# Kernel optimization log

Measured on AMD Instinct MI355X. Metric: run time of the kernel, lower is better.

Reference implementation:

```python
import jax, jax.numpy as jnp
import numpy as np

NUM_HEADS = 16


def setup_inputs() -> dict:
    key = jax.random.key(0)
    k1, k2, k3 = jax.random.split(key, 3)
    B, N, C = 4, 2048, 1024
    x = jax.random.normal(k1, (B, N, C), dtype=jnp.float32)
    w_qkv = jax.random.normal(k2, (C, 3 * C), dtype=jnp.float32) * (C ** -0.5)
    w_proj = jax.random.normal(k3, (C, C), dtype=jnp.float32) * (C ** -0.5)
    b_proj = jnp.zeros((C,), dtype=jnp.float32)
    return {"x": x, "w_qkv": w_qkv, "w_proj": w_proj, "b_proj": b_proj}


def reference(x, w_qkv, w_proj, b_proj):
    B, N, C = x.shape
    H = NUM_HEADS
    hd = C // H
    scale = hd ** -0.5
    # qkv projection (no bias), split into q, k, v per head
    qkv = jnp.einsum('bnc,cd->bnd', x, w_qkv)            # [B, N, 3C]
    qkv = qkv.reshape(B, N, 3, H, hd).transpose(0, 3, 2, 1, 4)  # [B, H, 3, N, hd]
    q, k, v = qkv[:, :, 0], qkv[:, :, 1], qkv[:, :, 2]   # each [B, H, N, hd]
    q = q * scale
    attn = jax.nn.softmax(jnp.einsum('bhnd,bhmd->bhnm', q, k), axis=-1)  # [B, H, N, N]
    out = jnp.einsum('bhnm,bhmd->bhnd', attn, v)         # [B, H, N, hd]
    out = out.transpose(0, 2, 1, 3).reshape(B, N, C)
    return jnp.einsum('bnc,cd->bnd', out, w_proj) + b_proj
```

## Files before the change

### kernel.cpp

```cpp
#include <hip/hip_runtime.h>

typedef short s16x8 __attribute__((ext_vector_type(8)));
typedef float f32x4 __attribute__((ext_vector_type(4)));
typedef float f32x16 __attribute__((ext_vector_type(16)));
typedef unsigned u32x4 __attribute__((ext_vector_type(4)));


__device__ __forceinline__ unsigned short bf16bits(float f) {
  unsigned u = __builtin_bit_cast(unsigned, f);
  unsigned rnd = 0x7FFFu + ((u >> 16) & 1u);
  return (unsigned short)((u + rnd) >> 16);
}

__device__ __forceinline__ unsigned pk_bf16(float lo, float hi) {
  unsigned r;
  asm("v_cvt_pk_bf16_f32 %0, %1, %2" : "=v"(r) : "v"(lo), "v"(hi));
  return r;
}

__device__ __forceinline__ void async16(const void* g, void* l) {
  __builtin_amdgcn_global_load_lds((const __attribute__((address_space(1))) void*)g,
                                   (__attribute__((address_space(3))) void*)l, 16, 0, 0);
}

__device__ __forceinline__ f32x4 mfma16(s16x8 a, s16x8 b, f32x4 c) {
  return __builtin_amdgcn_mfma_f32_16x16x32_bf16(a, b, c, 0, 0, 0);
}

__device__ __forceinline__ f32x16 mfma32(s16x8 a, s16x8 b, f32x16 c) {
  return __builtin_amdgcn_mfma_f32_32x32x16_bf16(a, b, c, 0, 0, 0);
}

__device__ __forceinline__ s16x8 lds_frag(const unsigned short* S, int row, int c8, int U) {
  int unit = row * U + (c8 ^ (row & (U - 1)));
  return *(const s16x8*)(S + unit * 8);
}


__global__ __launch_bounds__(256) void cvt_f32_bf16(const float4* __restrict__ in,
                                                    unsigned short* __restrict__ out, int n4) {
  int i = blockIdx.x * blockDim.x + threadIdx.x;
  int stride = gridDim.x * blockDim.x;
  for (; i < n4; i += stride) {
    float4 v = in[i];
    ushort4 o;
    o.x = bf16bits(v.x); o.y = bf16bits(v.y); o.z = bf16bits(v.z); o.w = bf16bits(v.w);
    *(ushort4*)(out + (size_t)i * 4) = o;
  }
}

__global__ __launch_bounds__(256) void transpose_f32_bf16(const float* __restrict__ in,
                                                          unsigned short* __restrict__ out,
                                                          int R, int C) {
  __shared__ float tile[32][33];
  int c0 = blockIdx.x * 32, r0 = blockIdx.y * 32;
  int tx = threadIdx.x, ty = threadIdx.y;
  #pragma unroll
  for (int i = 0; i < 32; i += 8)
    tile[ty + i][tx] = in[(size_t)(r0 + ty + i) * C + c0 + tx];
  __syncthreads();
  #pragma unroll
  for (int i = 0; i < 32; i += 8)
    out[(size_t)(c0 + ty + i) * R + r0 + tx] = bf16bits(tile[tx][ty + i]);
}


template <typename EPI>
__global__ __launch_bounds__(256) void gemm_bt(const unsigned short* __restrict__ A,
                                               const unsigned short* __restrict__ Bt,
                                               int K, EPI epi) {
  __shared__ __align__(16) unsigned short As[128 * 64];
  __shared__ __align__(16) unsigned short Bs[128 * 64];
  const int tid = threadIdx.x, wid = tid >> 6, lane = tid & 63;
  const int quad = lane >> 4, l16 = lane & 15;
  const int bm0 = blockIdx.y * 128, bn0 = blockIdx.x * 128;
  const int wm = (wid & 1) * 64, wn = (wid >> 1) * 64;
  f32x4 acc[4][4] = {};

  for (int kt = 0; kt < K; kt += 64) {
    #pragma unroll
    for (int t = 0; t < 4; ++t) {
      int c = wid * 4 + t;
      int u = c * 64 + lane;
      int row = u >> 3;
      int c8 = (u & 7) ^ (row & 7);
      async16(A + (size_t)(bm0 + row) * K + kt + c8 * 8, (char*)As + c * 1024);
      async16(Bt + (size_t)(bn0 + row) * K + kt + c8 * 8, (char*)Bs + c * 1024);
    }
    __syncthreads();
    #pragma unroll
    for (int kk = 0; kk < 2; ++kk) {
      s16x8 a[4], b[4];
      #pragma unroll
      for (int i = 0; i < 4; ++i) a[i] = lds_frag(As, wm + i * 16 + l16, kk * 4 + quad, 8);
      #pragma unroll
      for (int j = 0; j < 4; ++j) b[j] = lds_frag(Bs, wn + j * 16 + l16, kk * 4 + quad, 8);
      #pragma unroll
      for (int i = 0; i < 4; ++i)
        #pragma unroll
        for (int j = 0; j < 4; ++j)
          acc[i][j] = mfma16(a[i], b[j], acc[i][j]);
    }
    __syncthreads();
  }
  #pragma unroll
  for (int i = 0; i < 4; ++i)
    #pragma unroll
    for (int j = 0; j < 4; ++j) {
      int m0 = bm0 + wm + i * 16 + quad * 4;
      int n = bn0 + wn + j * 16 + l16;
      #pragma unroll
      for (int r = 0; r < 4; ++r) epi(m0 + r, n, acc[i][j][r]);
    }
}

struct QKVEpi {
  unsigned short *Q, *K, *Vt;
  float qscale;
  __device__ __forceinline__ void operator()(int m, int n, float v) const {
    int s = n >> 10, h = (n >> 6) & 15, d = n & 63;
    int b = m >> 11, ns = m & 2047;
    if (s == 2) {
      Vt[(((size_t)b * 16 + h) * 64 + d) * 2048 + ns] = bf16bits(v);
    } else {
      unsigned short* dst = s ? K : Q;
      float val = s ? v : v * qscale;
      dst[(((size_t)b * 16 + h) * 2048 + ns) * 64 + d] = bf16bits(val);
    }
  }
};

struct ProjEpi {
  const float* bias;
  float* out;
  __device__ __forceinline__ void operator()(int m, int n, float v) const {
    out[(size_t)m * 1024 + n] = v + bias[n];
  }
};

__global__ __launch_bounds__(256, 3) void flash_attn(const unsigned short* __restrict__ Q,
                                                     const unsigned short* __restrict__ K,
                                                     const unsigned short* __restrict__ Vt,
                                                     unsigned short* __restrict__ O) {
  __shared__ __align__(16) unsigned short Ks[2][64 * 64];
  __shared__ __align__(16) unsigned short Vs[2][64 * 64];
  const int tid = threadIdx.x, wid = tid >> 6, lane = tid & 63;
  const int l31 = lane & 31, half = lane >> 5;
  const int bh = blockIdx.y, qt = blockIdx.x;
  const unsigned short* Qg = Q + (size_t)bh * 2048 * 64;
  const unsigned short* Kg = K + (size_t)bh * 2048 * 64;
  const unsigned short* Vg = Vt + (size_t)bh * 64 * 2048;
  const int q0 = qt * 256 + wid * 64;

  s16x8 qB[2][4];
  #pragma unroll
  for (int g = 0; g < 2; ++g) {
    int qrow = q0 + g * 32 + l31;
    #pragma unroll
    for (int s = 0; s < 4; ++s)
      qB[g][s] = *(const s16x8*)&Qg[(size_t)qrow * 64 + s * 16 + half * 8];
  }

  const int c0 = wid * 2, c1 = wid * 2 + 1;
  const int u0 = c0 * 64 + lane, u1 = c1 * 64 + lane;
  const int kr0 = u0 >> 3, kc0 = ((u0 & 7) ^ (kr0 & 7)) * 8;
  const int kr1 = u1 >> 3, kc1 = ((u1 & 7) ^ (kr1 & 7)) * 8;

  auto stage = [&](int kt, int buf) {
    const int kb = kt * 64;
    async16(Kg + (size_t)(kb + kr0) * 64 + kc0, (char*)&Ks[buf][0] + c0 * 1024);
    async16(Kg + (size_t)(kb + kr1) * 64 + kc1, (char*)&Ks[buf][0] + c1 * 1024);
    async16(Vg + (size_t)kr0 * 2048 + kb + kc0, (char*)&Vs[buf][0] + c0 * 1024);
    async16(Vg + (size_t)kr1 * 2048 + kb + kc1, (char*)&Vs[buf][0] + c1 * 1024);
  };

  f32x16 oacc[2][2] = {};
  float l_i[2] = {0.f, 0.f};
  const f32x16 fz = {};

  stage(0, 0);
  for (int kt = 0; kt < 32; ++kt) {
    const int cur = kt & 1;
    __syncthreads();
    if (kt + 1 < 32) stage(kt + 1, cur ^ 1);
    const unsigned short* ks = &Ks[cur][0];
    const unsigned short* vs = &Vs[cur][0];

    #pragma unroll
    for (int kf = 0; kf < 2; ++kf) {
      f32x16 st[2];
      {
        s16x8 a = lds_frag(ks, kf * 32 + l31, half, 8);
        st[0] = mfma32(a, qB[0][0], fz);
        st[1] = mfma32(a, qB[1][0], fz);
      }
      #pragma unroll
      for (int s = 1; s < 4; ++s) {
        s16x8 a = lds_frag(ks, kf * 32 + l31, s * 2 + half, 8);
        st[0] = mfma32(a, qB[0][s], st[0]);
        st[1] = mfma32(a, qB[1][s], st[1]);
      }
      #pragma unroll
      for (int g = 0; g < 2; ++g) {
        float rs = 0.f;
        #pragma unroll
        for (int r = 0; r < 16; ++r) {
          float p = __builtin_amdgcn_exp2f(st[g][r]);
          st[g][r] = p;
          rs += p;
        }
        rs += __shfl_xor(rs, 32);
        l_i[g] += rs;
      }
      #pragma unroll
      for (int t = 0; t < 2; ++t) {
        int rb = t * 8;
        u32x4 bP[2];
        #pragma unroll
        for (int g = 0; g < 2; ++g) {
          unsigned pa0 = pk_bf16(st[g][rb + 0], st[g][rb + 1]);
          unsigned pa1 = pk_bf16(st[g][rb + 2], st[g][rb + 3]);
          unsigned pb0 = pk_bf16(st[g][rb + 4], st[g][rb + 5]);
          unsigned pb1 = pk_bf16(st[g][rb + 6], st[g][rb + 7]);
          unsigned s0 = half ? pa0 : pb0;
          unsigned s1 = half ? pa1 : pb1;
          unsigned r0 = (unsigned)__shfl_xor((int)s0, 32);
          unsigned r1 = (unsigned)__shfl_xor((int)s1, 32);
          bP[g][0] = half ? r0 : pa0;
          bP[g][1] = half ? r1 : pa1;
          bP[g][2] = half ? pb0 : r0;
          bP[g][3] = half ? pb1 : r1;
        }
        #pragma unroll
        for (int f = 0; f < 2; ++f) {
          s16x8 aV = lds_frag(vs, f * 32 + l31, (kf * 2 + t) * 2 + half, 8);
          oacc[0][f] = mfma32(aV, __builtin_bit_cast(s16x8, bP[0]), oacc[0][f]);
          oacc[1][f] = mfma32(aV, __builtin_bit_cast(s16x8, bP[1]), oacc[1][f]);
        }
      }
    }
  }

  const int b = bh >> 4, h = bh & 15;
  #pragma unroll
  for (int g = 0; g < 2; ++g) {
    float inv = 1.f / l_i[g];
    int qrow = q0 + g * 32 + l31;
    size_t base = (((size_t)b * 2048 + qrow) * 16 + h) * 64;
    #pragma unroll
    for (int f = 0; f < 2; ++f)
      #pragma unroll
      for (int q = 0; q < 4; ++q) {
        int d0 = f * 32 + q * 8 + half * 4;
        uint2 o;
        o.x = pk_bf16(oacc[g][f][q * 4 + 0] * inv, oacc[g][f][q * 4 + 1] * inv);
        o.y = pk_bf16(oacc[g][f][q * 4 + 2] * inv, oacc[g][f][q * 4 + 3] * inv);
        *(uint2*)&O[base + d0] = o;
      }
  }
}


extern "C" void kernel_launch(void* const* d_in, const int* in_sizes, int n_in,
                              void* d_out, int out_size, void* d_ws, size_t ws_size,
                              hipStream_t stream) {
  (void)in_sizes; (void)n_in; (void)out_size; (void)ws_size;
  const float* x = (const float*)d_in[0];
  const float* w_qkv = (const float*)d_in[1];
  const float* w_proj = (const float*)d_in[2];
  const float* b_proj = (const float*)d_in[3];
  float* out = (float*)d_out;
  char* ws = (char*)d_ws;
  const size_t MB = 1ull << 20;
  unsigned short* Xb  = (unsigned short*)(ws);
  unsigned short* Wqt = (unsigned short*)(ws + 16 * MB);
  unsigned short* Wpt = (unsigned short*)(ws + 22 * MB);
  unsigned short* Qb  = (unsigned short*)(ws + 24 * MB);
  unsigned short* Kb  = (unsigned short*)(ws + 40 * MB);
  unsigned short* Vt  = (unsigned short*)(ws + 56 * MB);
  unsigned short* Ob  = Xb;

  cvt_f32_bf16<<<2048, 256, 0, stream>>>((const float4*)x, Xb, 8388608 / 4);
  transpose_f32_bf16<<<dim3(96, 32), dim3(32, 8), 0, stream>>>(w_qkv, Wqt, 1024, 3072);
  transpose_f32_bf16<<<dim3(32, 32), dim3(32, 8), 0, stream>>>(w_proj, Wpt, 1024, 1024);

  QKVEpi e1{Qb, Kb, Vt, 0.125f * 1.44269504088896340736f};
  gemm_bt<QKVEpi><<<dim3(24, 64), 256, 0, stream>>>(Xb, Wqt, 1024, e1);

  flash_attn<<<dim3(8, 64), 256, 0, stream>>>(Qb, Kb, Vt, Ob);

  ProjEpi e2{b_proj, out};
  gemm_bt<ProjEpi><<<dim3(8, 64), 256, 0, stream>>>(Ob, Wpt, 1024, e2);
}
```

Measured before the change: 317.5 us.

## Swap GEMM operands for vectorized epilogue stores and transpose V separately

Swaps the A/B operands of both GEMMs so each lane's four accumulator values are contiguous along the output's fast dimension. The epilogues can then pack to bf16 and write 8-byte or 16-byte vector stores instead of scattered scalar ones. V is now written row-major, and a new small kernel transposes it through LDS into the Vt layout that flash attention expects. The input conversion also uses the packed bf16 convert instruction. The trade-off is an extra kernel launch and an extra pass over V in exchange for coalesced epilogue writes.

```diff
diff --git a/kernel.cpp b/kernel.cpp
--- a/kernel.cpp
+++ b/kernel.cpp
@@ -43,9 +43,10 @@
   int stride = gridDim.x * blockDim.x;
   for (; i < n4; i += stride) {
     float4 v = in[i];
-    ushort4 o;
-    o.x = bf16bits(v.x); o.y = bf16bits(v.y); o.z = bf16bits(v.z); o.w = bf16bits(v.w);
-    *(ushort4*)(out + (size_t)i * 4) = o;
+    uint2 o;
+    o.x = pk_bf16(v.x, v.y);
+    o.y = pk_bf16(v.z, v.w);
+    *(uint2*)(out + (size_t)i * 4) = o;
   }
 }
 
@@ -62,6 +63,29 @@
   #pragma unroll
   for (int i = 0; i < 32; i += 8)
     out[(size_t)(c0 + ty + i) * R + r0 + tx] = bf16bits(tile[tx][ty + i]);
+}
+
+__global__ __launch_bounds__(256) void transpose_v(const unsigned short* __restrict__ V,
+                                                   unsigned short* __restrict__ Vt) {
+  __shared__ unsigned short sm[64 * 68];
+  int bh = blockIdx.y, kt0 = blockIdx.x * 64;
+  const unsigned short* v = V + (size_t)bh * 2048 * 64 + (size_t)kt0 * 64;
+  unsigned short* vt = Vt + (size_t)bh * 64 * 2048;
+  int t = threadIdx.x;
+  #pragma unroll
+  for (int i = 0; i < 4; ++i) {
+    int u = i * 256 + t;
+    int f = u * 4;
+    int k = f >> 6, d0 = f & 63;
+    *(uint2*)&sm[k * 68 + d0] = *(const uint2*)&v[f];
+  }
+  __syncthreads();
+  #pragma unroll
+  for (int j = 0; j < 16; ++j) {
+    int o = j * 256 + t;
+    int d = o >> 6, k = o & 63;
+    vt[(size_t)d * 2048 + kt0 + k] = sm[k * 68 + d];
+  }
 }
 
 
@@ -106,35 +130,32 @@
   #pragma unroll
   for (int i = 0; i < 4; ++i)
     #pragma unroll
-    for (int j = 0; j < 4; ++j) {
-      int m0 = bm0 + wm + i * 16 + quad * 4;
-      int n = bn0 + wn + j * 16 + l16;
-      #pragma unroll
-      for (int r = 0; r < 4; ++r) epi(m0 + r, n, acc[i][j][r]);
-    }
+    for (int j = 0; j < 4; ++j)
+      epi.store4(bm0 + wm + i * 16 + quad * 4, bn0 + wn + j * 16 + l16, acc[i][j]);
 }
 
 struct QKVEpi {
-  unsigned short *Q, *K, *Vt;
+  unsigned short *Q, *K, *V;
   float qscale;
-  __device__ __forceinline__ void operator()(int m, int n, float v) const {
-    int s = n >> 10, h = (n >> 6) & 15, d = n & 63;
-    int b = m >> 11, ns = m & 2047;
-    if (s == 2) {
-      Vt[(((size_t)b * 16 + h) * 64 + d) * 2048 + ns] = bf16bits(v);
-    } else {
-      unsigned short* dst = s ? K : Q;
-      float val = s ? v : v * qscale;
-      dst[(((size_t)b * 16 + h) * 2048 + ns) * 64 + d] = bf16bits(val);
-    }
+  __device__ __forceinline__ void store4(int m0, int n, f32x4 v) const {
+    int s = m0 >> 10, h = (m0 >> 6) & 15, d = m0 & 63;
+    int b = n >> 11, ns = n & 2047;
+    unsigned short* dst = (s == 0) ? Q : ((s == 1) ? K : V);
+    float sc = (s == 0) ? qscale : 1.f;
+    uint2 o;
+    o.x = pk_bf16(v[0] * sc, v[1] * sc);
+    o.y = pk_bf16(v[2] * sc, v[3] * sc);
+    *(uint2*)&dst[(((size_t)b * 16 + h) * 2048 + ns) * 64 + d] = o;
   }
 };
 
 struct ProjEpi {
   const float* bias;
   float* out;
-  __device__ __forceinline__ void operator()(int m, int n, float v) const {
-    out[(size_t)m * 1024 + n] = v + bias[n];
+  __device__ __forceinline__ void store4(int m0, int n, f32x4 v) const {
+    float4 b4 = *(const float4*)&bias[m0];
+    float4 o = {v[0] + b4.x, v[1] + b4.y, v[2] + b4.z, v[3] + b4.w};
+    *(float4*)&out[(size_t)n * 1024 + m0] = o;
   }
 };
 
@@ -277,18 +298,20 @@
   unsigned short* Wpt = (unsigned short*)(ws + 22 * MB);
   unsigned short* Qb  = (unsigned short*)(ws + 24 * MB);
   unsigned short* Kb  = (unsigned short*)(ws + 40 * MB);
-  unsigned short* Vt  = (unsigned short*)(ws + 56 * MB);
-  unsigned short* Ob  = Xb;
+  unsigned short* Vb  = (unsigned short*)(ws + 56 * MB);
+  unsigned short* Vt  = Xb;
+  unsigned short* Ob  = Vb;
 
   cvt_f32_bf16<<<2048, 256, 0, stream>>>((const float4*)x, Xb, 8388608 / 4);
   transpose_f32_bf16<<<dim3(96, 32), dim3(32, 8), 0, stream>>>(w_qkv, Wqt, 1024, 3072);
   transpose_f32_bf16<<<dim3(32, 32), dim3(32, 8), 0, stream>>>(w_proj, Wpt, 1024, 1024);
 
-  QKVEpi e1{Qb, Kb, Vt, 0.125f * 1.44269504088896340736f};
-  gemm_bt<QKVEpi><<<dim3(24, 64), 256, 0, stream>>>(Xb, Wqt, 1024, e1);
-
+  QKVEpi e1{Qb, Kb, Vb, 0.125f * 1.44269504088896340736f};
+  gemm_bt<QKVEpi><<<dim3(64, 24), 256, 0, stream>>>(Wqt, Xb, 1024, e1);
+
+  transpose_v<<<dim3(32, 64), 256, 0, stream>>>(Vb, Vt);
   flash_attn<<<dim3(8, 64), 256, 0, stream>>>(Qb, Kb, Vt, Ob);
 
   ProjEpi e2{b_proj, out};
-  gemm_bt<ProjEpi><<<dim3(8, 64), 256, 0, stream>>>(Ob, Wpt, 1024, e2);
-}
+  gemm_bt<ProjEpi><<<dim3(64, 8), 256, 0, stream>>>(Wpt, Ob, 1024, e2);
+}
```

New measurement: 284.6 us. -10.3%, faster.
